# Kernel tuning notes

Hardware: AMD Instinct MI355X
Metric: run time of the kernel (lower is better)

Reference implementation:

```python
import jax, jax.numpy as jnp
import numpy as np

N = 50000   # nodes
E = 800000  # edges (avg degree 16)
D0 = 256    # input feat dim
H1, D1 = 4, 64  # layer1 heads, per-head dim
H2, D2 = 4, 64  # layer2 heads, per-head dim
NEG_SLOPE = 0.2


def setup_inputs() -> dict:
    key = jax.random.key(0)
    ks = jax.random.split(key, 9)
    s = 0.1
    feature = jax.random.normal(ks[0], (N, D0), jnp.float32)
    src = jax.random.randint(ks[1], (E,), 0, N, dtype=jnp.int32)
    dst = jax.random.randint(ks[2], (E,), 0, N, dtype=jnp.int32)
    W1 = jax.random.normal(ks[3], (D0, H1 * D1), jnp.float32) * s
    al1 = jax.random.normal(ks[4], (H1, D1), jnp.float32) * s
    ar1 = jax.random.normal(ks[5], (H1, D1), jnp.float32) * s
    W2 = jax.random.normal(ks[6], (H1 * D1, H2 * D2), jnp.float32) * s
    al2 = jax.random.normal(ks[7], (H2, D2), jnp.float32) * s
    ar2 = jax.random.normal(ks[8], (H2, D2), jnp.float32) * s
    return dict(feature=feature, W1=W1, al1=al1, ar1=ar1,
                W2=W2, al2=al2, ar2=ar2, src=src, dst=dst)


def gat_conv(x, W, al, ar, src, dst, H, d, act):
    # x: [N, in]; W: [in, H*d]; al, ar: [H, d]
    feat = (x @ W).reshape(N, H, d)                 # [N,H,d]
    el = jnp.einsum('nhd,hd->nh', feat, al)         # [N,H] src-side score
    er = jnp.einsum('nhd,hd->nh', feat, ar)         # [N,H] dst-side score
    e = jax.nn.leaky_relu(el[src] + er[dst], NEG_SLOPE)  # [E,H]
    # segment softmax over edges grouped by destination node
    m = jax.ops.segment_max(e, dst, num_segments=N)      # [N,H]
    ex = jnp.exp(e - m[dst])                             # [E,H]
    denom = jax.ops.segment_sum(ex, dst, num_segments=N) # [N,H]
    alpha = ex / jnp.maximum(denom[dst], 1e-9)           # [E,H]
    msg = feat[src] * alpha[..., None]                   # [E,H,d]
    out = jax.ops.segment_sum(msg, dst, num_segments=N)  # [N,H,d]
    return act(out)


def reference(feature, W1, al1, ar1, W2, al2, ar2, src, dst):
    h = gat_conv(feature, W1, al1, ar1, src, dst, H1, D1, jax.nn.elu)  # [N,H1,D1]
    h = h.reshape(N, H1 * D1)                                          # concat heads
    h = gat_conv(h, W2, al2, ar2, src, dst, H2, D2, lambda x: x)       # [N,H2,D2]
    return h.mean(axis=1)                                              # mean over heads -> [N,D2]
```

## Files before the change

### kernel.cpp

```cpp
#include <hip/hip_runtime.h>
#include <hip/hip_fp16.h>
#include <math.h>
#include <stdint.h>

#define NNODES 50000
#define NEDGES 800000
#define DIM 256
#define HEADS 4
#define DH 64
#define NEG_SLOPE 0.2f

#define CSR_NPB 1024
#define CSR_NB ((NNODES + CSR_NPB - 1) / CSR_NPB)

typedef _Float16 half8 __attribute__((ext_vector_type(8)));
typedef float floatx4 __attribute__((ext_vector_type(4)));

static __device__ __forceinline__ float h2f(unsigned short h) {
  __half x = *(const __half*)&h;
  return __half2float(x);
}
static __device__ __forceinline__ unsigned short f2h(float f) {
  __half x = __float2half(f);
  return *(const unsigned short*)&x;
}

__global__ __launch_bounds__(256) void wt_k(const float* __restrict__ W1,
                                            const float* __restrict__ W2,
                                            _Float16* __restrict__ WT1,
                                            _Float16* __restrict__ WT2) {
  int b = blockIdx.x;
  const float* W = (b < 256) ? W1 : W2;
  _Float16* WT = (b < 256) ? WT1 : WT2;
  int n = b & 255;
  int k = threadIdx.x;
  WT[n * 256 + k] = (_Float16)W[k * 256 + n];
}

template <typename AT>
__global__ __launch_bounds__(256) void gemm_k(const AT* __restrict__ A,
                                              const _Float16* __restrict__ BT,
                                              const float* __restrict__ alw,
                                              const float* __restrict__ arw,
                                              unsigned short* __restrict__ Cb,
                                              float* __restrict__ el,
                                              float* __restrict__ er, int M) {
  __shared__ __attribute__((aligned(16))) _Float16 Asl[64][40];
  __shared__ __attribute__((aligned(16))) _Float16 Bsl[256][40];
  int t = threadIdx.x;
  int lane = t & 63, w = t >> 6;
  int m16 = lane & 15, q = lane >> 4;
  int row0 = blockIdx.x * 64;
  floatx4 acc[4][4];
#pragma unroll
  for (int i = 0; i < 4; ++i)
#pragma unroll
    for (int j = 0; j < 4; ++j) acc[i][j] = (floatx4){0.f, 0.f, 0.f, 0.f};

  float4 alv[4], arv[4];
#pragma unroll
  for (int ni = 0; ni < 4; ++ni) {
    alv[ni] = *(const float4*)&alw[w * 64 + ni * 16 + q * 4];
    arv[ni] = *(const float4*)&arw[w * 64 + ni * 16 + q * 4];
  }

  int arow = t >> 2, akoff = (t & 3) * 8;

  for (int k0 = 0; k0 < DIM; k0 += 32) {
    if constexpr (sizeof(AT) == 4) {
      float4 x0 = make_float4(0.f, 0.f, 0.f, 0.f);
      float4 x1 = make_float4(0.f, 0.f, 0.f, 0.f);
      if (row0 + arow < M) {
        const float* ap = (const float*)&A[(size_t)(row0 + arow) * DIM + k0 + akoff];
        x0 = *(const float4*)ap;
        x1 = *(const float4*)(ap + 4);
      }
      half8 hv;
      hv[0] = (_Float16)x0.x; hv[1] = (_Float16)x0.y;
      hv[2] = (_Float16)x0.z; hv[3] = (_Float16)x0.w;
      hv[4] = (_Float16)x1.x; hv[5] = (_Float16)x1.y;
      hv[6] = (_Float16)x1.z; hv[7] = (_Float16)x1.w;
      *(half8*)&Asl[arow][akoff] = hv;
    } else {
      int4 x = make_int4(0, 0, 0, 0);
      if (row0 + arow < M)
        x = *(const int4*)&A[(size_t)(row0 + arow) * DIM + k0 + akoff];
      *(int4*)&Asl[arow][akoff] = x;
    }
    {
      const _Float16* bp = &BT[(size_t)t * 256 + k0];
      *(int4*)&Bsl[t][0] = *(const int4*)bp;
      *(int4*)&Bsl[t][8] = *(const int4*)(bp + 8);
      *(int4*)&Bsl[t][16] = *(const int4*)(bp + 16);
      *(int4*)&Bsl[t][24] = *(const int4*)(bp + 24);
    }
    __syncthreads();
    half8 wf[4], af[4];
#pragma unroll
    for (int i = 0; i < 4; ++i)
      wf[i] = *(const half8*)&Bsl[w * 64 + i * 16 + m16][q * 8];
#pragma unroll
    for (int i = 0; i < 4; ++i) af[i] = *(const half8*)&Asl[i * 16 + m16][q * 8];
#pragma unroll
    for (int mi = 0; mi < 4; ++mi)
#pragma unroll
      for (int ni = 0; ni < 4; ++ni)
        acc[mi][ni] = __builtin_amdgcn_mfma_f32_16x16x32_f16(
            wf[ni], af[mi], acc[mi][ni], 0, 0, 0);
    __syncthreads();
  }
#pragma unroll
  for (int mi = 0; mi < 4; ++mi) {
    int node = row0 + mi * 16 + m16;
    float pl = 0.f, pr = 0.f;
#pragma unroll
    for (int ni = 0; ni < 4; ++ni) {
      pl += acc[mi][ni][0] * alv[ni].x + acc[mi][ni][1] * alv[ni].y +
            acc[mi][ni][2] * alv[ni].z + acc[mi][ni][3] * alv[ni].w;
      pr += acc[mi][ni][0] * arv[ni].x + acc[mi][ni][1] * arv[ni].y +
            acc[mi][ni][2] * arv[ni].z + acc[mi][ni][3] * arv[ni].w;
    }
    pl += __shfl_xor(pl, 16, 64); pl += __shfl_xor(pl, 32, 64);
    pr += __shfl_xor(pr, 16, 64); pr += __shfl_xor(pr, 32, 64);
    if (q == 0 && node < M) {
      el[node * HEADS + w] = pl;
      er[node * HEADS + w] = pr;
    }
    if (node < M) {
#pragma unroll
      for (int ni = 0; ni < 4; ++ni) {
        ushort4 o;
        o.x = f2h(acc[mi][ni][0]); o.y = f2h(acc[mi][ni][1]);
        o.z = f2h(acc[mi][ni][2]); o.w = f2h(acc[mi][ni][3]);
        *(ushort4*)&Cb[(size_t)node * DIM + w * 64 + ni * 16 + q * 4] = o;
      }
    }
  }
}

__global__ __launch_bounds__(256) void deg_k(const int* __restrict__ dst,
                                             int* __restrict__ deg) {
  int e4 = (blockIdx.x * 256 + threadIdx.x) * 4;
  if (e4 < NEDGES) {
    int4 d = *(const int4*)&dst[e4];
    atomicAdd(&deg[d.x], 1);
    atomicAdd(&deg[d.y], 1);
    atomicAdd(&deg[d.z], 1);
    atomicAdd(&deg[d.w], 1);
  }
}

__global__ __launch_bounds__(256) void csr_part_k(const int* __restrict__ deg,
                                                  int* __restrict__ bsum) {
  __shared__ int ws[4];
  int t = threadIdx.x, lane = t & 63, w = t >> 6;
  int idx = blockIdx.x * CSR_NPB + t * 4;
  int s = 0;
  if (idx < NNODES) {
    int4 v = *(const int4*)&deg[idx];
    s = v.x + v.y + v.z + v.w;
  }
#pragma unroll
  for (int off = 1; off < 64; off <<= 1) s += __shfl_xor(s, off, 64);
  if (lane == 0) ws[w] = s;
  __syncthreads();
  if (t == 0) bsum[blockIdx.x] = ws[0] + ws[1] + ws[2] + ws[3];
}

__global__ __launch_bounds__(64) void csr_mid_k(const int* __restrict__ bsum,
                                                int* __restrict__ bbase,
                                                int* __restrict__ row_ptr) {
  int t = threadIdx.x;
  int v = (t < CSR_NB) ? bsum[t] : 0;
  int incl = v;
#pragma unroll
  for (int off = 1; off < 64; off <<= 1) {
    int u = __shfl_up(incl, off, 64);
    if (t >= off) incl += u;
  }
  if (t < CSR_NB) bbase[t] = incl - v;
  if (t == 0) row_ptr[NNODES] = NEDGES;
}

__global__ __launch_bounds__(256) void csr_emit_k(const int* __restrict__ deg,
                                                  const int* __restrict__ bbase,
                                                  int* __restrict__ row_ptr,
                                                  int* __restrict__ cursor) {
  __shared__ int ws[4];
  int t = threadIdx.x, lane = t & 63, w = t >> 6;
  int idx = blockIdx.x * CSR_NPB + t * 4;
  int4 v = make_int4(0, 0, 0, 0);
  if (idx < NNODES) v = *(const int4*)&deg[idx];
  int s0 = v.x, s1 = s0 + v.y, s2 = s1 + v.z, s3 = s2 + v.w;
  int incl = s3;
#pragma unroll
  for (int off = 1; off < 64; off <<= 1) {
    int u = __shfl_up(incl, off, 64);
    if (lane >= off) incl += u;
  }
  if (lane == 63) ws[w] = incl;
  __syncthreads();
  int wbase = 0;
#pragma unroll
  for (int i = 0; i < 4; ++i)
    if (i < w) wbase += ws[i];
  int base = bbase[blockIdx.x] + wbase + incl - s3;
  if (idx < NNODES) {
    int4 rp = make_int4(base, base + s0, base + s1, base + s2);
    *(int4*)&row_ptr[idx] = rp;
    *(int4*)&cursor[idx] = rp;
  }
}

__global__ __launch_bounds__(256) void scatter_k(const int* __restrict__ src,
                                                 const int* __restrict__ dst,
                                                 int* __restrict__ cursor,
                                                 int* __restrict__ srcoff) {
  int e4 = (blockIdx.x * 256 + threadIdx.x) * 4;
  if (e4 < NEDGES) {
    int4 s = *(const int4*)&src[e4];
    int4 d = *(const int4*)&dst[e4];
    int p;
    p = atomicAdd(&cursor[d.x], 1); srcoff[p] = s.x << 9;
    p = atomicAdd(&cursor[d.y], 1); srcoff[p] = s.y << 9;
    p = atomicAdd(&cursor[d.z], 1); srcoff[p] = s.z << 9;
    p = atomicAdd(&cursor[d.w], 1); srcoff[p] = s.w << 9;
  }
}

template <int MODE>
__global__ __launch_bounds__(256) void agg_k(const unsigned short* __restrict__ feat,
                                             const float* __restrict__ el,
                                             const float* __restrict__ er,
                                             const int* __restrict__ row_ptr,
                                             const int* __restrict__ srcoff,
                                             void* __restrict__ outp) {
  int lane = threadIdx.x & 63;
  int w = threadIdx.x >> 6;
  int n = blockIdx.x * 4 + w;
  if (n >= NNODES) return;
  int h = lane >> 4;
  int hsel = lane & 3;
  int esel = lane >> 2;
  int beg = row_ptr[n], end = row_ptr[n + 1];
  float erv = er[n * HEADS + hsel];
  int laneByte = lane * 8;
  const char* fb = (const char*)feat;
  const char* elb = (const char*)el;
  float a0 = 0.f, a1 = 0.f, a2 = 0.f, a3 = 0.f, sume = 0.f;
  for (int c0 = beg; c0 < end; c0 += 16) {
    int soff = 0;
    if (lane < 16 && c0 + lane < end) soff = srcoff[c0 + lane];
    float av = 0.f;
    if (c0 + esel < end) {
      int sE = __shfl(soff, esel, 64);
      float elv = *(const float*)(elb + (sE >> 5) + hsel * 4);
      float v = elv + erv;
      v = v > 0.f ? v : NEG_SLOPE * v;
      av = __expf(v);
    }
    for (int j4 = 0; j4 < 16; j4 += 4) {
      if (c0 + j4 >= end) break;
#pragma unroll
      for (int jj = 0; jj < 4; ++jj) {
        int j = j4 + jj;
        int sB = __shfl(soff, j, 64);
        float a = __shfl(av, 4 * j + h, 64);
        ushort4 u = *(const ushort4*)(fb + (sB + laneByte));
        a0 += h2f(u.x) * a;
        a1 += h2f(u.y) * a;
        a2 += h2f(u.z) * a;
        a3 += h2f(u.w) * a;
        sume += a;
      }
    }
  }
  float inv = 1.f / fmaxf(sume, 1e-9f);
  a0 *= inv; a1 *= inv; a2 *= inv; a3 *= inv;
  if (MODE == 1) {
    a0 = a0 > 0.f ? a0 : (__expf(a0) - 1.f);
    a1 = a1 > 0.f ? a1 : (__expf(a1) - 1.f);
    a2 = a2 > 0.f ? a2 : (__expf(a2) - 1.f);
    a3 = a3 > 0.f ? a3 : (__expf(a3) - 1.f);
    ushort4 o;
    o.x = f2h(a0); o.y = f2h(a1); o.z = f2h(a2); o.w = f2h(a3);
    *(ushort4*)((char*)outp + (size_t)n * 512 + laneByte) = o;
  } else {
    a0 += __shfl_xor(a0, 16, 64); a0 += __shfl_xor(a0, 32, 64);
    a1 += __shfl_xor(a1, 16, 64); a1 += __shfl_xor(a1, 32, 64);
    a2 += __shfl_xor(a2, 16, 64); a2 += __shfl_xor(a2, 32, 64);
    a3 += __shfl_xor(a3, 16, 64); a3 += __shfl_xor(a3, 32, 64);
    if (lane < 16) {
      float4 o = make_float4(a0 * 0.25f, a1 * 0.25f, a2 * 0.25f, a3 * 0.25f);
      *(float4*)((float*)outp + (size_t)n * 64 + lane * 4) = o;
    }
  }
}

extern "C" void kernel_launch(void* const* d_in, const int* in_sizes, int n_in,
                              void* d_out, int out_size, void* d_ws, size_t ws_size,
                              hipStream_t stream) {
  const float* feature = (const float*)d_in[0];
  const float* W1 = (const float*)d_in[1];
  const float* al1 = (const float*)d_in[2];
  const float* ar1 = (const float*)d_in[3];
  const float* W2 = (const float*)d_in[4];
  const float* al2 = (const float*)d_in[5];
  const float* ar2 = (const float*)d_in[6];
  const int* src = (const int*)d_in[7];
  const int* dst = (const int*)d_in[8];
  float* out = (float*)d_out;

  uintptr_t p = (uintptr_t)d_ws;
  auto alloc = [&](size_t bytes) -> void* {
    uintptr_t cur = (p + 255) & ~(uintptr_t)255;
    p = cur + bytes;
    return (void*)cur;
  };
  unsigned short* featH = (unsigned short*)alloc((size_t)NNODES * DIM * 2);
  unsigned short* hidH  = (unsigned short*)alloc((size_t)NNODES * DIM * 2);
  _Float16* WT1 = (_Float16*)alloc((size_t)256 * 256 * 2);
  _Float16* WT2 = (_Float16*)alloc((size_t)256 * 256 * 2);
  float* el    = (float*)alloc((size_t)NNODES * HEADS * 4);
  float* er    = (float*)alloc((size_t)NNODES * HEADS * 4);
  int* deg     = (int*)alloc((size_t)NNODES * 4);
  int* row_ptr = (int*)alloc((size_t)(NNODES + 1) * 4);
  int* cursor  = (int*)alloc((size_t)NNODES * 4);
  int* srcoff  = (int*)alloc((size_t)NEDGES * 4);
  int* bsum    = (int*)alloc((size_t)CSR_NB * 4);
  int* bbase   = (int*)alloc((size_t)CSR_NB * 4);

  const int E4B = (NEDGES / 4 + 255) / 256;
  const int MB = (NNODES + 63) / 64;
  const int AB = (NNODES + 3) / 4;

  wt_k<<<512, 256, 0, stream>>>(W1, W2, WT1, WT2);
  hipMemsetAsync(deg, 0, (size_t)NNODES * 4, stream);
  deg_k<<<E4B, 256, 0, stream>>>(dst, deg);
  csr_part_k<<<CSR_NB, 256, 0, stream>>>(deg, bsum);
  csr_mid_k<<<1, 64, 0, stream>>>(bsum, bbase, row_ptr);
  csr_emit_k<<<CSR_NB, 256, 0, stream>>>(deg, bbase, row_ptr, cursor);
  scatter_k<<<E4B, 256, 0, stream>>>(src, dst, cursor, srcoff);

  gemm_k<float><<<MB, 256, 0, stream>>>(feature, WT1, al1, ar1, featH, el, er, NNODES);
  agg_k<1><<<AB, 256, 0, stream>>>(featH, el, er, row_ptr, srcoff, hidH);

  gemm_k<_Float16><<<MB, 256, 0, stream>>>((const _Float16*)hidH, WT2, al2, ar2,
                                           featH, el, er, NNODES);
  agg_k<2><<<AB, 256, 0, stream>>>(featH, el, er, row_ptr, srcoff, out);
}
```

Before: 367.6 us.

## Load GEMM MFMA fragments directly from global and fully unroll edge aggregation

The GEMM kernel stops staging A and B tiles through shared memory with two barriers per k-step. Each lane now loads its MFMA fragments straight from global memory, with row indices clamped instead of zero-filled, and the k-loop is fully unrolled. The aggregation kernel replaces its early-exit inner loop with a fully unrolled 16-edge loop; out-of-range edges read offset 0 with weight 0, so there are no branches. The trade-off is redundant global/L2 traffic, since each wave re-reads A and four waves share no B reuse. The aggregation path also issues wasted loads for partial edge chunks.

New measurement: 401.0 us. +9.1%, slower.

```diff
diff --git a/kernel.cpp b/kernel.cpp
--- a/kernel.cpp
+++ b/kernel.cpp
@@ -45,8 +45,6 @@
                                               unsigned short* __restrict__ Cb,
                                               float* __restrict__ el,
                                               float* __restrict__ er, int M) {
-  __shared__ __attribute__((aligned(16))) _Float16 Asl[64][40];
-  __shared__ __attribute__((aligned(16))) _Float16 Bsl[256][40];
   int t = threadIdx.x;
   int lane = t & 63, w = t >> 6;
   int m16 = lane & 15, q = lane >> 4;
@@ -64,51 +62,44 @@
     arv[ni] = *(const float4*)&arw[w * 64 + ni * 16 + q * 4];
   }
 
-  int arow = t >> 2, akoff = (t & 3) * 8;
-
+  const AT* ab[4];
+  const _Float16* bb[4];
+#pragma unroll
+  for (int i = 0; i < 4; ++i) {
+    int ar = row0 + i * 16 + m16;
+    if (ar > M - 1) ar = M - 1;
+    ab[i] = &A[(size_t)ar * DIM + q * 8];
+    bb[i] = &BT[(size_t)(w * 64 + i * 16 + m16) * DIM + q * 8];
+  }
+
+#pragma unroll
   for (int k0 = 0; k0 < DIM; k0 += 32) {
-    if constexpr (sizeof(AT) == 4) {
-      float4 x0 = make_float4(0.f, 0.f, 0.f, 0.f);
-      float4 x1 = make_float4(0.f, 0.f, 0.f, 0.f);
-      if (row0 + arow < M) {
-        const float* ap = (const float*)&A[(size_t)(row0 + arow) * DIM + k0 + akoff];
-        x0 = *(const float4*)ap;
-        x1 = *(const float4*)(ap + 4);
+    half8 wf[4], af[4];
+#pragma unroll
+    for (int i = 0; i < 4; ++i) wf[i] = *(const half8*)(bb[i] + k0);
+#pragma unroll
+    for (int i = 0; i < 4; ++i) {
+      if constexpr (sizeof(AT) == 4) {
+        float4 x0 = *(const float4*)(ab[i] + k0);
+        float4 x1 = *(const float4*)(ab[i] + k0 + 4);
+        half8 hv;
+        hv[0] = (_Float16)x0.x; hv[1] = (_Float16)x0.y;
+        hv[2] = (_Float16)x0.z; hv[3] = (_Float16)x0.w;
+        hv[4] = (_Float16)x1.x; hv[5] = (_Float16)x1.y;
+        hv[6] = (_Float16)x1.z; hv[7] = (_Float16)x1.w;
+        af[i] = hv;
+      } else {
+        af[i] = *(const half8*)(ab[i] + k0);
       }
-      half8 hv;
-      hv[0] = (_Float16)x0.x; hv[1] = (_Float16)x0.y;
-      hv[2] = (_Float16)x0.z; hv[3] = (_Float16)x0.w;
-      hv[4] = (_Float16)x1.x; hv[5] = (_Float16)x1.y;
-      hv[6] = (_Float16)x1.z; hv[7] = (_Float16)x1.w;
-      *(half8*)&Asl[arow][akoff] = hv;
-    } else {
-      int4 x = make_int4(0, 0, 0, 0);
-      if (row0 + arow < M)
-        x = *(const int4*)&A[(size_t)(row0 + arow) * DIM + k0 + akoff];
-      *(int4*)&Asl[arow][akoff] = x;
-    }
-    {
-      const _Float16* bp = &BT[(size_t)t * 256 + k0];
-      *(int4*)&Bsl[t][0] = *(const int4*)bp;
-      *(int4*)&Bsl[t][8] = *(const int4*)(bp + 8);
-      *(int4*)&Bsl[t][16] = *(const int4*)(bp + 16);
-      *(int4*)&Bsl[t][24] = *(const int4*)(bp + 24);
-    }
-    __syncthreads();
-    half8 wf[4], af[4];
-#pragma unroll
-    for (int i = 0; i < 4; ++i)
-      wf[i] = *(const half8*)&Bsl[w * 64 + i * 16 + m16][q * 8];
-#pragma unroll
-    for (int i = 0; i < 4; ++i) af[i] = *(const half8*)&Asl[i * 16 + m16][q * 8];
+    }
 #pragma unroll
     for (int mi = 0; mi < 4; ++mi)
 #pragma unroll
       for (int ni = 0; ni < 4; ++ni)
         acc[mi][ni] = __builtin_amdgcn_mfma_f32_16x16x32_f16(
             wf[ni], af[mi], acc[mi][ni], 0, 0, 0);
-    __syncthreads();
-  }
+  }
+
 #pragma unroll
   for (int mi = 0; mi < 4; ++mi) {
     int node = row0 + mi * 16 + m16;
@@ -259,20 +250,16 @@
       v = v > 0.f ? v : NEG_SLOPE * v;
       av = __expf(v);
     }
-    for (int j4 = 0; j4 < 16; j4 += 4) {
-      if (c0 + j4 >= end) break;
-#pragma unroll
-      for (int jj = 0; jj < 4; ++jj) {
-        int j = j4 + jj;
-        int sB = __shfl(soff, j, 64);
-        float a = __shfl(av, 4 * j + h, 64);
-        ushort4 u = *(const ushort4*)(fb + (sB + laneByte));
-        a0 += h2f(u.x) * a;
-        a1 += h2f(u.y) * a;
-        a2 += h2f(u.z) * a;
-        a3 += h2f(u.w) * a;
-        sume += a;
-      }
+#pragma unroll
+    for (int j = 0; j < 16; ++j) {
+      int sB = __shfl(soff, j, 64);
+      float a = __shfl(av, 4 * j + h, 64);
+      ushort4 u = *(const ushort4*)(fb + (sB + laneByte));
+      a0 += h2f(u.x) * a;
+      a1 += h2f(u.y) * a;
+      a2 += h2f(u.z) * a;
+      a3 += h2f(u.w) * a;
+      sume += a;
     }
   }
   float inv = 1.f / fmaxf(sume, 1e-9f);
```
